# Kernel tuning notes

Hardware: AMD Instinct MI355X
Metric: run time of the kernel (lower is better)

## Reference

```python
import jax, jax.numpy as jnp
import numpy as np

N_NODES = 50000
N_EDGES = 800000
D_FEAT = 64
UNITS = 64


def setup_inputs() -> dict:
    key = jax.random.key(0)
    k1, k2, k3, k4, k5 = jax.random.split(key, 5)
    embeddings = jax.random.normal(k1, (N_NODES, D_FEAT), dtype=jnp.float32)
    edge_src = jax.random.randint(k2, (N_EDGES,), 0, N_NODES, dtype=jnp.int32)
    edge_dst = jax.random.randint(k3, (N_EDGES,), 0, N_NODES, dtype=jnp.int32)
    # normalized-adjacency-like positive weights
    edge_w = jax.random.uniform(k4, (N_EDGES,), dtype=jnp.float32)
    # keras 'truncated_normal' initializer default stddev=0.05 (approx w/ normal)
    kernel = jax.random.normal(k5, (D_FEAT, UNITS), dtype=jnp.float32) * 0.05
    return {"embeddings": embeddings, "edge_src": edge_src,
            "edge_dst": edge_dst, "edge_w": edge_w, "kernel": kernel}


def reference(embeddings, edge_src, edge_dst, edge_w, kernel):
    # SpMM: agg[i] = sum_{e: dst(e)=i} w_e * embeddings[src(e)]
    msgs = embeddings[edge_src] * edge_w[:, None]            # [E, D]
    agg = jax.ops.segment_sum(msgs, edge_dst,
                              num_segments=embeddings.shape[0])  # [N, D]
    # dense GEMM + relu (use_bias=False)
    return jax.nn.relu(agg @ kernel)                          # [N, units]
```

## Files before the change

kernel.cpp:

```cpp
#include <hip/hip_runtime.h>
#include <hip/hip_bf16.h>

#define D    64
#define CH   4096
#define PASS 2048

__global__ __launch_bounds__(256) void gemm_part(
    const float* __restrict__ emb,
    const float* __restrict__ W,
    __hip_bfloat16* __restrict__ Zb,
    const int*   __restrict__ dst,
    int*         __restrict__ histG,
    ushort*      __restrict__ lrank,
    int N, int E, int NB, int gemmTiles)
{
    __shared__ int smem[4096];

    if ((int)blockIdx.x >= gemmTiles) {
        const int c  = (int)blockIdx.x - gemmTiles;
        const int t  = threadIdx.x;
        for (int b = t; b < NB; b += 256) smem[b] = 0;
        __syncthreads();
        const int e0 = c * CH;
#pragma unroll
        for (int i = 0; i < 16; ++i) {
            int e = e0 + i * 256 + t;
            if (e < E) {
                int b = dst[e] >> 6;
                lrank[e] = (ushort)atomicAdd(&smem[b], 1);
            }
        }
        __syncthreads();
        for (int b = t; b < NB; b += 256)
            histG[(size_t)c * NB + b] = smem[b];
        return;
    }

    const int lane = threadIdx.x & 63;
    const int wave = threadIdx.x >> 6;

    float wcol[D];
#pragma unroll
    for (int k = 0; k < D; ++k) wcol[k] = W[k * D + lane];

    float* At = (float*)smem;
    const int row0 = blockIdx.x * 64;

    for (int i = threadIdx.x; i < 1024; i += 256) {
        int r  = i >> 4;
        int gr = row0 + r;
        float4 v;
        if (gr < N) v = reinterpret_cast<const float4*>(emb)[(size_t)gr * 16 + (i & 15)];
        else        v = float4{0.f, 0.f, 0.f, 0.f};
        reinterpret_cast<float4*>(At)[i] = v;
    }
    __syncthreads();

    for (int rr = 0; rr < 16; ++rr) {
        int r  = wave * 16 + rr;
        int gr = row0 + r;
        if (gr >= N) break;
        const float4* arow = reinterpret_cast<const float4*>(At + r * D);
        float acc = 0.f;
#pragma unroll
        for (int k4 = 0; k4 < 16; ++k4) {
            float4 a = arow[k4];
            acc = fmaf(a.x, wcol[4 * k4 + 0], acc);
            acc = fmaf(a.y, wcol[4 * k4 + 1], acc);
            acc = fmaf(a.z, wcol[4 * k4 + 2], acc);
            acc = fmaf(a.w, wcol[4 * k4 + 3], acc);
        }
        Zb[(size_t)gr * D + lane] = __float2bfloat16(acc);
    }
}

__global__ __launch_bounds__(256) void scan_hist(
    const int* __restrict__ histG, int* __restrict__ offsets,
    int* __restrict__ partials, int NB, int NC, int M)
{
    __shared__ int sh[256];
    const int t    = threadIdx.x;
    const int base = blockIdx.x * 4096 + t * 16;

    int v[16], ps[16];
    int b = base / NC, c = base - b * NC;
#pragma unroll
    for (int k = 0; k < 16; ++k) {
        int m = base + k;
        v[k] = (m < M) ? histG[(size_t)c * NB + b] : 0;
        if (++c == NC) { c = 0; ++b; }
    }
    int s = 0;
#pragma unroll
    for (int k = 0; k < 16; ++k) { ps[k] = s; s += v[k]; }
    sh[t] = s;
    __syncthreads();
    for (int off = 1; off < 256; off <<= 1) {
        int x = (t >= off) ? sh[t - off] : 0;
        __syncthreads();
        sh[t] += x;
        __syncthreads();
    }
    const int excl = sh[t] - s;
#pragma unroll
    for (int k = 0; k < 4; ++k) {
        int4 o;
        o.x = excl + ps[4*k+0]; o.y = excl + ps[4*k+1];
        o.z = excl + ps[4*k+2]; o.w = excl + ps[4*k+3];
        reinterpret_cast<int4*>(offsets + base)[k] = o;
    }
    if (t == 255) partials[blockIdx.x] = sh[255];
}

__device__ __forceinline__ void scan_partials_lds256(
    const int* __restrict__ partials, int nb, int* sp)
{
    const int t    = threadIdx.x;
    const int orig = (t < nb) ? partials[t] : 0;
    sp[t] = orig;
    __syncthreads();
    for (int off = 1; off < 256; off <<= 1) {
        int x = (t >= off) ? sp[t - off] : 0;
        __syncthreads();
        sp[t] += x;
        __syncthreads();
    }
    int incl = sp[t];
    __syncthreads();
    sp[t] = incl - orig;
    __syncthreads();
}

__global__ __launch_bounds__(256) void scatter_bkt(
    const int*    __restrict__ src,
    const int*    __restrict__ dst,
    const float*  __restrict__ w,
    const ushort* __restrict__ lrank,
    const int*    __restrict__ histG,
    const int*    __restrict__ offsets,
    const int*    __restrict__ partials,
    int2*         __restrict__ csr,
    int E, int NB, int NC, int nb2)
{
    __shared__ int2   rec[CH];
    __shared__ ushort bidv[CH];
    __shared__ int    delta[784];
    __shared__ int    sh[256];
    __shared__ int    sp[256];
    scan_partials_lds256(partials, nb2, sp);

    const int t  = threadIdx.x;
    const int c  = blockIdx.x;
    const int e0 = c * CH;
    const int cnt = min(CH, E - e0);

    int hv[4], hps[4];
    const int hbase = t * 4;
#pragma unroll
    for (int k = 0; k < 4; ++k) {
        int b = hbase + k;
        hv[k] = (b < NB) ? histG[(size_t)c * NB + b] : 0;
    }
    int s = 0;
#pragma unroll
    for (int k = 0; k < 4; ++k) { hps[k] = s; s += hv[k]; }
    sh[t] = s;
    __syncthreads();
    for (int off = 1; off < 256; off <<= 1) {
        int x = (t >= off) ? sh[t - off] : 0;
        __syncthreads();
        sh[t] += x;
        __syncthreads();
    }
    const int hexcl = sh[t] - s;
#pragma unroll
    for (int k = 0; k < 4; ++k) {
        int b = hbase + k;
        if (b < NB) delta[b] = hexcl + hps[k];
    }
    __syncthreads();

#pragma unroll
    for (int i = 0; i < 16; ++i) {
        int e = e0 + i * 256 + t;
        if (e < E) {
            int d  = dst[e];
            int b  = d >> 6;
            int lp = delta[b] + lrank[e];
            rec[lp]  = make_int2(src[e] | ((d & 63) << 16), __float_as_int(w[e]));
            bidv[lp] = (ushort)b;
        }
    }
    __syncthreads();

#pragma unroll
    for (int k = 0; k < 4; ++k) {
        int b = hbase + k;
        if (b < NB) {
            int m = b * NC + c;
            delta[b] = offsets[m] + sp[m >> 12] - delta[b];
        }
    }
    __syncthreads();

    for (int j = t; j < cnt; j += 256)
        csr[j + delta[bidv[j]]] = rec[j];
}

__global__ __launch_bounds__(256) void aggregate(
    const __hip_bfloat16* __restrict__ Zb,
    const int2* __restrict__ csr,
    const int*  __restrict__ offsets,
    const int*  __restrict__ partials,
    float*      __restrict__ out,
    int N, int E, int NB, int NC, int nb2)
{
    __shared__ int2 srec[PASS];
    __shared__ int  hist[64];
    __shared__ int  nbase[65];
    __shared__ int  sp[256];
    scan_partials_lds256(partials, nb2, sp);

    const int t = threadIdx.x;
    const int b = blockIdx.x;

    const int m0 = b * NC;
    const int bStart = offsets[m0] + sp[m0 >> 12];
    int bEnd;
    if (b + 1 < NB) { int m1 = (b + 1) * NC; bEnd = offsets[m1] + sp[m1 >> 12]; }
    else            bEnd = E;

    const int wv   = t >> 6;
    const int lane = t & 63;
    const int slot = lane >> 4;
    const int q    = lane & 15;

    const ushort4* Zu = reinterpret_cast<const ushort4*>(Zb);

    float4 acc[16];
#pragma unroll
    for (int r = 0; r < 16; ++r) acc[r] = float4{0.f, 0.f, 0.f, 0.f};

    for (int cur = bStart; cur < bEnd; cur += PASS) {
        const int cnt = min(PASS, bEnd - cur);

        if (t < 64) hist[t] = 0;
        __syncthreads();

        int2 myrec[8]; int mypos[8];
#pragma unroll
        for (int k = 0; k < 8; ++k) {
            int j = k * 256 + t;
            if (j < cnt) {
                int2 r2 = csr[cur + j];
                myrec[k] = r2;
                mypos[k] = atomicAdd(&hist[(r2.x >> 16) & 63], 1);
            }
        }
        __syncthreads();

        if (t < 64) {
            int v = hist[t];
            int x = v;
            for (int off = 1; off < 64; off <<= 1) {
                int y = __shfl_up(x, off, 64);
                if (t >= off) x += y;
            }
            nbase[t] = x - v;
            if (t == 63) nbase[64] = x;
        }
        __syncthreads();

#pragma unroll
        for (int k = 0; k < 8; ++k) {
            int j = k * 256 + t;
            if (j < cnt)
                srec[nbase[(myrec[k].x >> 16) & 63] + mypos[k]] = myrec[k];
        }
        __syncthreads();

        for (int r = 0; r < 16; ++r) {
            const int nl = wv * 16 + r;
            const int je = nbase[nl + 1];
            for (int j = nbase[nl] + slot; j < je; j += 4) {
                int2   e  = srec[j];
                float  ww = __int_as_float(e.y);
                int    sn = e.x & 0xFFFF;
                ushort4 zu = Zu[(size_t)sn * 16 + q];
                acc[r].x = fmaf(ww, __uint_as_float((unsigned)zu.x << 16), acc[r].x);
                acc[r].y = fmaf(ww, __uint_as_float((unsigned)zu.y << 16), acc[r].y);
                acc[r].z = fmaf(ww, __uint_as_float((unsigned)zu.z << 16), acc[r].z);
                acc[r].w = fmaf(ww, __uint_as_float((unsigned)zu.w << 16), acc[r].w);
            }
        }
        __syncthreads();
    }

    const int node0 = (b << 6) + wv * 16;
#pragma unroll
    for (int r = 0; r < 16; ++r) {
        float4 a = acc[r];
#pragma unroll
        for (int off = 32; off >= 16; off >>= 1) {
            a.x += __shfl_down(a.x, off, 64);
            a.y += __shfl_down(a.y, off, 64);
            a.z += __shfl_down(a.z, off, 64);
            a.w += __shfl_down(a.w, off, 64);
        }
        int node = node0 + r;
        if (lane < 16 && node < N) {
            float4 o;
            o.x = fmaxf(a.x, 0.f);
            o.y = fmaxf(a.y, 0.f);
            o.z = fmaxf(a.z, 0.f);
            o.w = fmaxf(a.w, 0.f);
            reinterpret_cast<float4*>(out)[(size_t)node * 16 + lane] = o;
        }
    }
}

extern "C" void kernel_launch(void* const* d_in, const int* in_sizes, int n_in,
                              void* d_out, int out_size, void* d_ws, size_t ws_size,
                              hipStream_t stream)
{
    const float* emb  = (const float*)d_in[0];
    const int*   esrc = (const int*)  d_in[1];
    const int*   edst = (const int*)  d_in[2];
    const float* ew   = (const float*)d_in[3];
    const float* W    = (const float*)d_in[4];
    float*       out  = (float*)d_out;

    const int N  = in_sizes[0] / D;
    const int E  = in_sizes[1];

    const int NB  = (N + 63) / 64;
    const int NC  = (E + CH - 1) / CH;
    const int M   = NB * NC;
    const int nb2 = (M + 4095) / 4096;
    const int Mpad = nb2 * 4096;

    char* p = (char*)d_ws;
    __hip_bfloat16* Zb = (__hip_bfloat16*)p;  p += (size_t)N * D * 2;
    int*    histG   = (int*)p;                p += (size_t)Mpad * 4;
    int*    offsets = (int*)p;                p += (size_t)Mpad * 4;
    int*    partials= (int*)p;                p += 256 * 4;
    ushort* lrank   = (ushort*)p;             p += (size_t)((E + 7) & ~7) * 2;
    int2*   csr     = (int2*)p;

    const int gemmTiles = (N + 63) / 64;
    gemm_part<<<gemmTiles + NC, 256, 0, stream>>>(
        emb, W, Zb, edst, histG, lrank, N, E, NB, gemmTiles);

    scan_hist<<<nb2, 256, 0, stream>>>(histG, offsets, partials, NB, NC, M);

    scatter_bkt<<<NC, 256, 0, stream>>>(
        esrc, edst, ew, lrank, histG, offsets, partials, csr, E, NB, NC, nb2);

    aggregate<<<NB, 256, 0, stream>>>(
        Zb, csr, offsets, partials, out, N, E, NB, NC, nb2);
}
```

Measured before the change: 145.5 us.

## Halve aggregation bucket size and widen per-lane bf16 gathers to 16 bytes

```diff
diff --git a/kernel.cpp b/kernel.cpp
--- a/kernel.cpp
+++ b/kernel.cpp
@@ -3,7 +3,8 @@
 
 #define D    64
 #define CH   4096
-#define PASS 2048
+#define BKT  32
+#define PASS 1024
 
 __global__ __launch_bounds__(256) void gemm_part(
     const float* __restrict__ emb,
@@ -26,7 +27,7 @@
         for (int i = 0; i < 16; ++i) {
             int e = e0 + i * 256 + t;
             if (e < E) {
-                int b = dst[e] >> 6;
+                int b = dst[e] / BKT;
                 lrank[e] = (ushort)atomicAdd(&smem[b], 1);
             }
         }
@@ -144,7 +145,7 @@
 {
     __shared__ int2   rec[CH];
     __shared__ ushort bidv[CH];
-    __shared__ int    delta[784];
+    __shared__ int    delta[1568];
     __shared__ int    sh[256];
     __shared__ int    sp[256];
     scan_partials_lds256(partials, nb2, sp);
@@ -154,16 +155,16 @@
     const int e0 = c * CH;
     const int cnt = min(CH, E - e0);
 
-    int hv[4], hps[4];
-    const int hbase = t * 4;
-#pragma unroll
-    for (int k = 0; k < 4; ++k) {
+    int hv[7], hps[7];
+    const int hbase = t * 7;
+#pragma unroll
+    for (int k = 0; k < 7; ++k) {
         int b = hbase + k;
         hv[k] = (b < NB) ? histG[(size_t)c * NB + b] : 0;
     }
     int s = 0;
 #pragma unroll
-    for (int k = 0; k < 4; ++k) { hps[k] = s; s += hv[k]; }
+    for (int k = 0; k < 7; ++k) { hps[k] = s; s += hv[k]; }
     sh[t] = s;
     __syncthreads();
     for (int off = 1; off < 256; off <<= 1) {
@@ -174,7 +175,7 @@
     }
     const int hexcl = sh[t] - s;
 #pragma unroll
-    for (int k = 0; k < 4; ++k) {
+    for (int k = 0; k < 7; ++k) {
         int b = hbase + k;
         if (b < NB) delta[b] = hexcl + hps[k];
     }
@@ -185,16 +186,16 @@
         int e = e0 + i * 256 + t;
         if (e < E) {
             int d  = dst[e];
-            int b  = d >> 6;
+            int b  = d / BKT;
             int lp = delta[b] + lrank[e];
-            rec[lp]  = make_int2(src[e] | ((d & 63) << 16), __float_as_int(w[e]));
+            rec[lp]  = make_int2(src[e] | ((d & (BKT - 1)) << 16), __float_as_int(w[e]));
             bidv[lp] = (ushort)b;
         }
     }
     __syncthreads();
 
 #pragma unroll
-    for (int k = 0; k < 4; ++k) {
+    for (int k = 0; k < 7; ++k) {
         int b = hbase + k;
         if (b < NB) {
             int m = b * NC + c;
@@ -216,8 +217,8 @@
     int N, int E, int NB, int NC, int nb2)
 {
     __shared__ int2 srec[PASS];
-    __shared__ int  hist[64];
-    __shared__ int  nbase[65];
+    __shared__ int  hist[BKT];
+    __shared__ int  nbase[BKT + 1];
     __shared__ int  sp[256];
     scan_partials_lds256(partials, nb2, sp);
 
@@ -232,89 +233,99 @@
 
     const int wv   = t >> 6;
     const int lane = t & 63;
-    const int slot = lane >> 4;
-    const int q    = lane & 15;
-
-    const ushort4* Zu = reinterpret_cast<const ushort4*>(Zb);
-
-    float4 acc[16];
-#pragma unroll
-    for (int r = 0; r < 16; ++r) acc[r] = float4{0.f, 0.f, 0.f, 0.f};
+    const int slot = lane >> 3;
+    const int q    = lane & 7;
+
+    const int4* Zq = reinterpret_cast<const int4*>(Zb);
+
+    float4 alo[8], ahi[8];
+#pragma unroll
+    for (int r = 0; r < 8; ++r) { alo[r] = float4{0,0,0,0}; ahi[r] = float4{0,0,0,0}; }
 
     for (int cur = bStart; cur < bEnd; cur += PASS) {
         const int cnt = min(PASS, bEnd - cur);
 
-        if (t < 64) hist[t] = 0;
-        __syncthreads();
-
-        int2 myrec[8]; int mypos[8];
-#pragma unroll
-        for (int k = 0; k < 8; ++k) {
+        if (t < BKT) hist[t] = 0;
+        __syncthreads();
+
+        int2 myrec[4]; int mypos[4];
+#pragma unroll
+        for (int k = 0; k < 4; ++k) {
             int j = k * 256 + t;
             if (j < cnt) {
                 int2 r2 = csr[cur + j];
                 myrec[k] = r2;
-                mypos[k] = atomicAdd(&hist[(r2.x >> 16) & 63], 1);
+                mypos[k] = atomicAdd(&hist[(r2.x >> 16) & (BKT - 1)], 1);
             }
         }
         __syncthreads();
 
-        if (t < 64) {
+        if (t < BKT) {
             int v = hist[t];
             int x = v;
-            for (int off = 1; off < 64; off <<= 1) {
+            for (int off = 1; off < BKT; off <<= 1) {
                 int y = __shfl_up(x, off, 64);
                 if (t >= off) x += y;
             }
             nbase[t] = x - v;
-            if (t == 63) nbase[64] = x;
-        }
-        __syncthreads();
-
-#pragma unroll
-        for (int k = 0; k < 8; ++k) {
+            if (t == BKT - 1) nbase[BKT] = x;
+        }
+        __syncthreads();
+
+#pragma unroll
+        for (int k = 0; k < 4; ++k) {
             int j = k * 256 + t;
             if (j < cnt)
-                srec[nbase[(myrec[k].x >> 16) & 63] + mypos[k]] = myrec[k];
-        }
-        __syncthreads();
-
-        for (int r = 0; r < 16; ++r) {
-            const int nl = wv * 16 + r;
+                srec[nbase[(myrec[k].x >> 16) & (BKT - 1)] + mypos[k]] = myrec[k];
+        }
+        __syncthreads();
+
+        for (int r = 0; r < 8; ++r) {
+            const int nl = wv * 8 + r;
             const int je = nbase[nl + 1];
-            for (int j = nbase[nl] + slot; j < je; j += 4) {
-                int2   e  = srec[j];
-                float  ww = __int_as_float(e.y);
-                int    sn = e.x & 0xFFFF;
-                ushort4 zu = Zu[(size_t)sn * 16 + q];
-                acc[r].x = fmaf(ww, __uint_as_float((unsigned)zu.x << 16), acc[r].x);
-                acc[r].y = fmaf(ww, __uint_as_float((unsigned)zu.y << 16), acc[r].y);
-                acc[r].z = fmaf(ww, __uint_as_float((unsigned)zu.z << 16), acc[r].z);
-                acc[r].w = fmaf(ww, __uint_as_float((unsigned)zu.w << 16), acc[r].w);
+            for (int j = nbase[nl] + slot; j < je; j += 8) {
+                int2  e  = srec[j];
+                float ww = __int_as_float(e.y);
+                int   sn = e.x & 0xFFFF;
+                int4  zz = Zq[(size_t)sn * 8 + q];
+                alo[r].x = fmaf(ww, __uint_as_float((unsigned)zz.x << 16),          alo[r].x);
+                alo[r].y = fmaf(ww, __uint_as_float((unsigned)zz.x & 0xFFFF0000u),  alo[r].y);
+                alo[r].z = fmaf(ww, __uint_as_float((unsigned)zz.y << 16),          alo[r].z);
+                alo[r].w = fmaf(ww, __uint_as_float((unsigned)zz.y & 0xFFFF0000u),  alo[r].w);
+                ahi[r].x = fmaf(ww, __uint_as_float((unsigned)zz.z << 16),          ahi[r].x);
+                ahi[r].y = fmaf(ww, __uint_as_float((unsigned)zz.z & 0xFFFF0000u),  ahi[r].y);
+                ahi[r].z = fmaf(ww, __uint_as_float((unsigned)zz.w << 16),          ahi[r].z);
+                ahi[r].w = fmaf(ww, __uint_as_float((unsigned)zz.w & 0xFFFF0000u),  ahi[r].w);
             }
         }
         __syncthreads();
     }
 
-    const int node0 = (b << 6) + wv * 16;
-#pragma unroll
-    for (int r = 0; r < 16; ++r) {
-        float4 a = acc[r];
-#pragma unroll
-        for (int off = 32; off >= 16; off >>= 1) {
-            a.x += __shfl_down(a.x, off, 64);
-            a.y += __shfl_down(a.y, off, 64);
-            a.z += __shfl_down(a.z, off, 64);
-            a.w += __shfl_down(a.w, off, 64);
+    const int node0 = b * BKT + wv * 8;
+#pragma unroll
+    for (int r = 0; r < 8; ++r) {
+        float4 lo = alo[r], hi = ahi[r];
+#pragma unroll
+        for (int off = 32; off >= 8; off >>= 1) {
+            lo.x += __shfl_down(lo.x, off, 64);
+            lo.y += __shfl_down(lo.y, off, 64);
+            lo.z += __shfl_down(lo.z, off, 64);
+            lo.w += __shfl_down(lo.w, off, 64);
+            hi.x += __shfl_down(hi.x, off, 64);
+            hi.y += __shfl_down(hi.y, off, 64);
+            hi.z += __shfl_down(hi.z, off, 64);
+            hi.w += __shfl_down(hi.w, off, 64);
         }
         int node = node0 + r;
-        if (lane < 16 && node < N) {
-            float4 o;
-            o.x = fmaxf(a.x, 0.f);
-            o.y = fmaxf(a.y, 0.f);
-            o.z = fmaxf(a.z, 0.f);
-            o.w = fmaxf(a.w, 0.f);
-            reinterpret_cast<float4*>(out)[(size_t)node * 16 + lane] = o;
+        if (lane < 8 && node < N) {
+            float4 o0, o1;
+            o0.x = fmaxf(lo.x, 0.f); o0.y = fmaxf(lo.y, 0.f);
+            o0.z = fmaxf(lo.z, 0.f); o0.w = fmaxf(lo.w, 0.f);
+            o1.x = fmaxf(hi.x, 0.f); o1.y = fmaxf(hi.y, 0.f);
+            o1.z = fmaxf(hi.z, 0.f); o1.w = fmaxf(hi.w, 0.f);
+            float4* orow = reinterpret_cast<float4*>(out) + (size_t)node * 16 + lane * 2;
+            orow[0] = o0;
+            orow[1] = o1;
         }
     }
 }
@@ -333,7 +344,7 @@
     const int N  = in_sizes[0] / D;
     const int E  = in_sizes[1];
 
-    const int NB  = (N + 63) / 64;
+    const int NB  = (N + BKT - 1) / BKT;
     const int NC  = (E + CH - 1) / CH;
     const int M   = NB * NC;
     const int nb2 = (M + 4095) / 4096;
```

New measurement: 147.4 us. Within noise of the previous version (+1.3%).
